# Performance work log

Measured on AMD Instinct MI355X. Metric: run time of the kernel, lower is better.

Reference implementation:

```python
import jax, jax.numpy as jnp
import numpy as np

N_NODES = 100000
N_EDGES = 3200000
D_IN = 256
D_OUT = 256


def setup_inputs() -> dict:
    key = jax.random.key(0)
    k1, k2, k3, k4, k5, k6 = jax.random.split(key, 6)
    x = jax.random.normal(k1, (N_NODES, D_IN), dtype=jnp.float32)
    edge_src = jax.random.randint(k2, (N_EDGES,), 0, N_NODES, dtype=jnp.int32)
    edge_dst = jax.random.randint(k3, (N_EDGES,), 0, N_NODES, dtype=jnp.int32)
    edge_weight = jax.random.uniform(k4, (N_EDGES,), dtype=jnp.float32)
    weight = jax.random.normal(k5, (D_IN, D_OUT), dtype=jnp.float32) * 0.02
    bias = jax.random.uniform(k6, (D_OUT,), dtype=jnp.float32)
    return {"x": x, "edge_src": edge_src, "edge_dst": edge_dst,
            "edge_weight": edge_weight, "weight": weight, "bias": bias}


def reference(x, edge_src, edge_dst, edge_weight, weight, bias):
    # support = X @ W  (dense GEMM)
    support = x @ weight  # [N, D_OUT]
    # output = A @ support, A given as COO edges (dst <- src with weight)
    msgs = support[edge_src] * edge_weight[:, None]  # [E, D_OUT]
    out = jax.ops.segment_sum(msgs, edge_dst, num_segments=N_NODES)  # [N, D_OUT]
    return out + bias
```

## Files before the change

### kernel.cpp

```cpp
#include <hip/hip_runtime.h>
#include <hip/hip_bf16.h>

#define N_NODES 100000
#define N_EDGES 3200000
#define DDIM    256
#define M_PAD   100096
#define NBKT    782
#define BCAP    4608
#define EPB_A   4096

typedef __attribute__((ext_vector_type(8))) short short8;
typedef __attribute__((ext_vector_type(4))) float f32x4;

typedef const __attribute__((address_space(1))) void gvoid_t;
typedef __attribute__((address_space(3))) void lvoid_t;

__device__ __forceinline__ void load_lds16(const void* g, void* l) {
  __builtin_amdgcn_global_load_lds((gvoid_t*)g, (lvoid_t*)l, 16, 0, 0);
}

__device__ __forceinline__ unsigned short f2bf(float f) {
  __hip_bfloat16 h = __float2bfloat16(f);
  return *(unsigned short*)&h;
}
__device__ __forceinline__ float bflo(unsigned u) { return __uint_as_float(u << 16); }
__device__ __forceinline__ float bfhi(unsigned u) { return __uint_as_float(u & 0xffff0000u); }

__global__ void conv_x_kernel(const float* __restrict__ x, unsigned short* __restrict__ xb) {
  size_t i = (size_t)blockIdx.x * blockDim.x + threadIdx.x;
  size_t idx = i * 4;
  if (idx >= (size_t)N_NODES * DDIM) return;
  float4 v = *(const float4*)(x + idx);
  ushort4 o;
  o.x = f2bf(v.x); o.y = f2bf(v.y); o.z = f2bf(v.z); o.w = f2bf(v.w);
  *(ushort4*)(xb + idx) = o;
}

__global__ void conv_w_kernel(const float* __restrict__ w, unsigned short* __restrict__ wt) {
  int t = blockIdx.x * blockDim.x + threadIdx.x;
  int n = t >> 8, k = t & 255;
  wt[t] = f2bf(w[k * 256 + n]);
}

__global__ __launch_bounds__(256) void gemm_kernel(const unsigned short* __restrict__ xb,
                                                   const unsigned short* __restrict__ wt,
                                                   unsigned short* __restrict__ sup) {
  __shared__ unsigned short As[128 * 32];
  __shared__ unsigned short Bs[128 * 32];
  const int tid  = threadIdx.x;
  const int w    = tid >> 6;
  const int lane = tid & 63;
  const int quad = lane >> 4;
  const int l15  = lane & 15;
  const int wr   = w >> 1, wc = w & 1;
  const int m0 = blockIdx.x * 128;
  const int n0 = blockIdx.y * 128;

  f32x4 acc[4][4] = {};

  const int srow   = lane >> 2;
  const int schunk = (lane & 3) * 8;

  for (int kt = 0; kt < 256; kt += 32) {
#pragma unroll
    for (int i = 0; i < 2; ++i) {
      int r = w * 32 + i * 16 + srow;
      load_lds16(xb + ((size_t)(m0 + r) * 256 + kt + schunk),
                 As + (w * 32 + i * 16) * 32);
      load_lds16(wt + ((size_t)(n0 + r) * 256 + kt + schunk),
                 Bs + (w * 32 + i * 16) * 32);
    }
    __syncthreads();

    short8 a[4], b[4];
#pragma unroll
    for (int mi = 0; mi < 4; ++mi)
      a[mi] = *(const short8*)(As + (wr * 64 + mi * 16 + l15) * 32 + quad * 8);
#pragma unroll
    for (int ni = 0; ni < 4; ++ni)
      b[ni] = *(const short8*)(Bs + (wc * 64 + ni * 16 + l15) * 32 + quad * 8);

#pragma unroll
    for (int mi = 0; mi < 4; ++mi)
#pragma unroll
      for (int ni = 0; ni < 4; ++ni)
        acc[mi][ni] = __builtin_amdgcn_mfma_f32_16x16x32_bf16(a[mi], b[ni], acc[mi][ni], 0, 0, 0);
    __syncthreads();
  }

#pragma unroll
  for (int mi = 0; mi < 4; ++mi) {
#pragma unroll
    for (int r = 0; r < 4; ++r) {
      size_t row = (size_t)(m0 + wr * 64 + mi * 16 + quad * 4 + r);
#pragma unroll
      for (int ni = 0; ni < 4; ++ni) {
        int col = n0 + wc * 64 + ni * 16 + l15;
        sup[row * 256 + col] = f2bf(acc[mi][ni][r]);
      }
    }
  }
}

__global__ __launch_bounds__(256) void binA_kernel(const int* __restrict__ src,
                                                   const int* __restrict__ dst,
                                                   const float* __restrict__ wgt,
                                                   int* __restrict__ gcur,
                                                   unsigned long long* __restrict__ region) {
  __shared__ unsigned long long staged[EPB_A];
  __shared__ unsigned short sbkt[EPB_A];
  __shared__ int lhist[NBKT];
  __shared__ int lstart[NBKT];
  __shared__ int lcur[NBKT];
  __shared__ int gb[NBKT];
  __shared__ int csum[256];

  const int t = threadIdx.x;
  const int e0 = blockIdx.x * EPB_A;
  const int ecnt = min(EPB_A, N_EDGES - e0);

  for (int i = t; i < NBKT; i += 256) lhist[i] = 0;
  __syncthreads();
  for (int k = t; k < ecnt; k += 256)
    atomicAdd(&lhist[dst[e0 + k] >> 7], 1);
  __syncthreads();

  int i0 = 4 * t;
  int a0 = (i0 + 0 < NBKT) ? lhist[i0 + 0] : 0;
  int a1 = (i0 + 1 < NBKT) ? lhist[i0 + 1] : 0;
  int a2 = (i0 + 2 < NBKT) ? lhist[i0 + 2] : 0;
  int a3 = (i0 + 3 < NBKT) ? lhist[i0 + 3] : 0;
  int s = a0 + a1 + a2 + a3;
  csum[t] = s;
  __syncthreads();
  for (int off = 1; off < 256; off <<= 1) {
    int v = (t >= off) ? csum[t - off] : 0;
    __syncthreads();
    csum[t] += v;
    __syncthreads();
  }
  int base = csum[t] - s;
  if (i0 + 0 < NBKT) lstart[i0 + 0] = base; base += a0;
  if (i0 + 1 < NBKT) lstart[i0 + 1] = base; base += a1;
  if (i0 + 2 < NBKT) lstart[i0 + 2] = base; base += a2;
  if (i0 + 3 < NBKT) lstart[i0 + 3] = base;
  __syncthreads();

  for (int i = t; i < NBKT; i += 256) {
    int c = lhist[i];
    int off = c ? atomicAdd(&gcur[i], c) : 0;
    gb[i] = i * BCAP + off;
    lcur[i] = lstart[i];
  }
  __syncthreads();

  for (int k = t; k < ecnt; k += 256) {
    int d  = dst[e0 + k];
    int sr = src[e0 + k];
    float w = wgt[e0 + k];
    int b = d >> 7;
    int p = atomicAdd(&lcur[b], 1);
    staged[p] = ((unsigned long long)__float_as_uint(w) << 32) |
                ((unsigned)(d & 127) << 17) | (unsigned)sr;
    sbkt[p] = (unsigned short)b;
  }
  __syncthreads();

  for (int j = t; j < ecnt; j += 256) {
    int b = sbkt[j];
    int addr = gb[b] + (j - lstart[b]);
    if (addr < (b + 1) * BCAP) region[addr] = staged[j];
  }
}

__global__ __launch_bounds__(256) void csrB_kernel(unsigned long long* __restrict__ region,
                                                   const int* __restrict__ gcur,
                                                   int2* __restrict__ rowse) {
  __shared__ unsigned long long lcsr[BCAP];
  __shared__ int lhist[128], loff[128], lcur[128];
  const int t = threadIdx.x;
  const int b = blockIdx.x;
  const int cnt = min(gcur[b], BCAP);
  const int base = b * BCAP;

  if (t < 128) lhist[t] = 0;
  __syncthreads();
  for (int j = t; j < cnt; j += 256) {
    unsigned lo = (unsigned)(region[base + j] & 0xffffffffu);
    atomicAdd(&lhist[(lo >> 17) & 127], 1);
  }
  __syncthreads();
  if (t < 128) loff[t] = lhist[t];
  __syncthreads();
  for (int off = 1; off < 128; off <<= 1) {
    int v = (t >= off && t < 128) ? loff[t - off] : 0;
    __syncthreads();
    if (t < 128) loff[t] += v;
    __syncthreads();
  }
  if (t < 128) { loff[t] -= lhist[t]; lcur[t] = loff[t]; }
  __syncthreads();
  for (int j = t; j < cnt; j += 256) {
    unsigned long long e = region[base + j];
    int dl = (int)((e >> 17) & 127);
    int p = atomicAdd(&lcur[dl], 1);
    lcsr[p] = e;
  }
  __syncthreads();
  for (int j = t; j < cnt; j += 256) region[base + j] = lcsr[j];
  if (t < 128) {
    int gd = b * 128 + t;
    if (gd < N_NODES) rowse[gd] = make_int2(base + loff[t], base + lcur[t]);
  }
}

__global__ __launch_bounds__(64) void gather_kernel(const unsigned long long* __restrict__ packed,
                                                    const int2* __restrict__ rowse,
                                                    const unsigned short* __restrict__ sup,
                                                    const float* __restrict__ bias,
                                                    float* __restrict__ out) {
  int n = blockIdx.x;
  int l = threadIdx.x;
  int c0 = l * 4;
  int2 se = rowse[n];
  int start = se.x, end = se.y;
  float4 bv = *(const float4*)(bias + c0);
  float a0 = bv.x, a1 = bv.y, a2 = bv.z, a3 = bv.w;

  int i = start;
  for (; i + 2 <= end; i += 2) {
    unsigned long long m0 = packed[i];
    unsigned long long m1 = packed[i + 1];
    int   s0 = (int)(m0 & 0x1ffffu);
    float w0 = __uint_as_float((unsigned)(m0 >> 32));
    int   s1 = (int)(m1 & 0x1ffffu);
    float w1 = __uint_as_float((unsigned)(m1 >> 32));
    uint2 p0 = *(const uint2*)(sup + (size_t)s0 * 256 + c0);
    uint2 p1 = *(const uint2*)(sup + (size_t)s1 * 256 + c0);
    a0 = fmaf(w0, bflo(p0.x), a0);
    a1 = fmaf(w0, bfhi(p0.x), a1);
    a2 = fmaf(w0, bflo(p0.y), a2);
    a3 = fmaf(w0, bfhi(p0.y), a3);
    a0 = fmaf(w1, bflo(p1.x), a0);
    a1 = fmaf(w1, bfhi(p1.x), a1);
    a2 = fmaf(w1, bflo(p1.y), a2);
    a3 = fmaf(w1, bfhi(p1.y), a3);
  }
  if (i < end) {
    unsigned long long m0 = packed[i];
    int   s0 = (int)(m0 & 0x1ffffu);
    float w0 = __uint_as_float((unsigned)(m0 >> 32));
    uint2 p0 = *(const uint2*)(sup + (size_t)s0 * 256 + c0);
    a0 = fmaf(w0, bflo(p0.x), a0);
    a1 = fmaf(w0, bfhi(p0.x), a1);
    a2 = fmaf(w0, bflo(p0.y), a2);
    a3 = fmaf(w0, bfhi(p0.y), a3);
  }
  *(float4*)(out + (size_t)n * 256 + c0) = make_float4(a0, a1, a2, a3);
}

extern "C" void kernel_launch(void* const* d_in, const int* in_sizes, int n_in,
                              void* d_out, int out_size, void* d_ws, size_t ws_size,
                              hipStream_t stream) {
  const float* x        = (const float*)d_in[0];
  const int*   edge_src = (const int*)d_in[1];
  const int*   edge_dst = (const int*)d_in[2];
  const float* edge_w   = (const float*)d_in[3];
  const float* weight   = (const float*)d_in[4];
  const float* bias     = (const float*)d_in[5];
  float* out = (float*)d_out;

  char* ws = (char*)d_ws;
  size_t off = 0;
  auto alloc = [&](size_t bytes) -> void* {
    void* p = ws + off;
    off = (off + bytes + 255) & ~(size_t)255;
    return p;
  };

  unsigned short* xb  = (unsigned short*)alloc((size_t)M_PAD * 256 * 2);
  unsigned short* wt  = (unsigned short*)alloc(256 * 256 * 2);
  unsigned short* sup = (unsigned short*)alloc((size_t)M_PAD * 256 * 2);

  char* xbb = (char*)xb;
  unsigned long long* region = (unsigned long long*)xbb;
  int*  gcur  = (int*)(xbb + (29u << 20));
  int2* rowse = (int2*)(xbb + (30u << 20));

  conv_x_kernel<<<25000, 256, 0, stream>>>(x, xb);
  conv_w_kernel<<<256, 256, 0, stream>>>(weight, wt);
  gemm_kernel<<<dim3(782, 2), 256, 0, stream>>>(xb, wt, sup);
  hipMemsetAsync(gcur, 0, NBKT * 4, stream);
  binA_kernel<<<(N_EDGES + EPB_A - 1) / EPB_A, 256, 0, stream>>>(edge_src, edge_dst, edge_w,
                                                                 gcur, region);
  csrB_kernel<<<NBKT, 256, 0, stream>>>(region, gcur, rowse);
  gather_kernel<<<N_NODES, 64, 0, stream>>>(region, rowse, sup, bias, out);
}
```

Baseline: 532.8 us.

## Fuse per-bucket CSR sort with the neighbor gather using the LDS-resident edge list

Merges the CSR bucket sort and the gather into one kernel with 512-thread blocks. Each block sorts its bucket's edges in LDS, then its 8 waves each aggregate 16 destination nodes straight from the LDS-sorted list. This drops the sorted-edge write-back, the row start/end array, one kernel launch and the global re-read of edges. The cost is a much smaller grid (782 blocks instead of 100k single-wave blocks), which may lower latency hiding for the random support reads and add load imbalance across waves.

Result: no change. 531.1 us (-0.3%).

```diff
diff --git a/kernel.cpp b/kernel.cpp
--- a/kernel.cpp
+++ b/kernel.cpp
@@ -8,6 +8,7 @@
 #define NBKT    782
 #define BCAP    4608
 #define EPB_A   4096
+#define GT      512
 
 typedef __attribute__((ext_vector_type(8))) short short8;
 typedef __attribute__((ext_vector_type(4))) float f32x4;
@@ -173,9 +174,12 @@
   }
 }
 
-__global__ __launch_bounds__(256) void csrB_kernel(unsigned long long* __restrict__ region,
-                                                   const int* __restrict__ gcur,
-                                                   int2* __restrict__ rowse) {
+__global__ __launch_bounds__(GT) void csr_gather_kernel(
+    const unsigned long long* __restrict__ region,
+    const int* __restrict__ gcur,
+    const unsigned short* __restrict__ sup,
+    const float* __restrict__ bias,
+    float* __restrict__ out) {
   __shared__ unsigned long long lcsr[BCAP];
   __shared__ int lhist[128], loff[128], lcur[128];
   const int t = threadIdx.x;
@@ -185,7 +189,7 @@
 
   if (t < 128) lhist[t] = 0;
   __syncthreads();
-  for (int j = t; j < cnt; j += 256) {
+  for (int j = t; j < cnt; j += GT) {
     unsigned lo = (unsigned)(region[base + j] & 0xffffffffu);
     atomicAdd(&lhist[(lo >> 17) & 127], 1);
   }
@@ -200,63 +204,56 @@
   }
   if (t < 128) { loff[t] -= lhist[t]; lcur[t] = loff[t]; }
   __syncthreads();
-  for (int j = t; j < cnt; j += 256) {
+  for (int j = t; j < cnt; j += GT) {
     unsigned long long e = region[base + j];
     int dl = (int)((e >> 17) & 127);
     int p = atomicAdd(&lcur[dl], 1);
     lcsr[p] = e;
   }
   __syncthreads();
-  for (int j = t; j < cnt; j += 256) region[base + j] = lcsr[j];
-  if (t < 128) {
-    int gd = b * 128 + t;
-    if (gd < N_NODES) rowse[gd] = make_int2(base + loff[t], base + lcur[t]);
-  }
-}
-
-__global__ __launch_bounds__(64) void gather_kernel(const unsigned long long* __restrict__ packed,
-                                                    const int2* __restrict__ rowse,
-                                                    const unsigned short* __restrict__ sup,
-                                                    const float* __restrict__ bias,
-                                                    float* __restrict__ out) {
-  int n = blockIdx.x;
-  int l = threadIdx.x;
-  int c0 = l * 4;
-  int2 se = rowse[n];
-  int start = se.x, end = se.y;
+
+  const int wv = t >> 6;
+  const int c0 = (t & 63) * 4;
   float4 bv = *(const float4*)(bias + c0);
-  float a0 = bv.x, a1 = bv.y, a2 = bv.z, a3 = bv.w;
-
-  int i = start;
-  for (; i + 2 <= end; i += 2) {
-    unsigned long long m0 = packed[i];
-    unsigned long long m1 = packed[i + 1];
-    int   s0 = (int)(m0 & 0x1ffffu);
-    float w0 = __uint_as_float((unsigned)(m0 >> 32));
-    int   s1 = (int)(m1 & 0x1ffffu);
-    float w1 = __uint_as_float((unsigned)(m1 >> 32));
-    uint2 p0 = *(const uint2*)(sup + (size_t)s0 * 256 + c0);
-    uint2 p1 = *(const uint2*)(sup + (size_t)s1 * 256 + c0);
-    a0 = fmaf(w0, bflo(p0.x), a0);
-    a1 = fmaf(w0, bfhi(p0.x), a1);
-    a2 = fmaf(w0, bflo(p0.y), a2);
-    a3 = fmaf(w0, bfhi(p0.y), a3);
-    a0 = fmaf(w1, bflo(p1.x), a0);
-    a1 = fmaf(w1, bfhi(p1.x), a1);
-    a2 = fmaf(w1, bflo(p1.y), a2);
-    a3 = fmaf(w1, bfhi(p1.y), a3);
-  }
-  if (i < end) {
-    unsigned long long m0 = packed[i];
-    int   s0 = (int)(m0 & 0x1ffffu);
-    float w0 = __uint_as_float((unsigned)(m0 >> 32));
-    uint2 p0 = *(const uint2*)(sup + (size_t)s0 * 256 + c0);
-    a0 = fmaf(w0, bflo(p0.x), a0);
-    a1 = fmaf(w0, bfhi(p0.x), a1);
-    a2 = fmaf(w0, bflo(p0.y), a2);
-    a3 = fmaf(w0, bfhi(p0.y), a3);
-  }
-  *(float4*)(out + (size_t)n * 256 + c0) = make_float4(a0, a1, a2, a3);
+
+  for (int dl = wv; dl < 128; dl += 8) {
+    int node = b * 128 + dl;
+    if (node >= N_NODES) continue;
+    int start = loff[dl];
+    int end   = lcur[dl];
+    float a0 = bv.x, a1 = bv.y, a2 = bv.z, a3 = bv.w;
+
+    int i = start;
+    for (; i + 2 <= end; i += 2) {
+      unsigned long long m0 = lcsr[i];
+      unsigned long long m1 = lcsr[i + 1];
+      int   s0 = (int)(m0 & 0x1ffffu);
+      float w0 = __uint_as_float((unsigned)(m0 >> 32));
+      int   s1 = (int)(m1 & 0x1ffffu);
+      float w1 = __uint_as_float((unsigned)(m1 >> 32));
+      uint2 p0 = *(const uint2*)(sup + (size_t)s0 * 256 + c0);
+      uint2 p1 = *(const uint2*)(sup + (size_t)s1 * 256 + c0);
+      a0 = fmaf(w0, bflo(p0.x), a0);
+      a1 = fmaf(w0, bfhi(p0.x), a1);
+      a2 = fmaf(w0, bflo(p0.y), a2);
+      a3 = fmaf(w0, bfhi(p0.y), a3);
+      a0 = fmaf(w1, bflo(p1.x), a0);
+      a1 = fmaf(w1, bfhi(p1.x), a1);
+      a2 = fmaf(w1, bflo(p1.y), a2);
+      a3 = fmaf(w1, bfhi(p1.y), a3);
+    }
+    if (i < end) {
+      unsigned long long m0 = lcsr[i];
+      int   s0 = (int)(m0 & 0x1ffffu);
+      float w0 = __uint_as_float((unsigned)(m0 >> 32));
+      uint2 p0 = *(const uint2*)(sup + (size_t)s0 * 256 + c0);
+      a0 = fmaf(w0, bflo(p0.x), a0);
+      a1 = fmaf(w0, bfhi(p0.x), a1);
+      a2 = fmaf(w0, bflo(p0.y), a2);
+      a3 = fmaf(w0, bfhi(p0.y), a3);
+    }
+    *(float4*)(out + (size_t)node * 256 + c0) = make_float4(a0, a1, a2, a3);
+  }
 }
 
 extern "C" void kernel_launch(void* const* d_in, const int* in_sizes, int n_in,
@@ -285,7 +282,6 @@
   char* xbb = (char*)xb;
   unsigned long long* region = (unsigned long long*)xbb;
   int*  gcur  = (int*)(xbb + (29u << 20));
-  int2* rowse = (int2*)(xbb + (30u << 20));
 
   conv_x_kernel<<<25000, 256, 0, stream>>>(x, xb);
   conv_w_kernel<<<256, 256, 0, stream>>>(weight, wt);
@@ -293,6 +289,5 @@
   hipMemsetAsync(gcur, 0, NBKT * 4, stream);
   binA_kernel<<<(N_EDGES + EPB_A - 1) / EPB_A, 256, 0, stream>>>(edge_src, edge_dst, edge_w,
                                                                  gcur, region);
-  csrB_kernel<<<NBKT, 256, 0, stream>>>(region, gcur, rowse);
-  gather_kernel<<<N_NODES, 64, 0, stream>>>(region, rowse, sup, bias, out);
-}
+  csr_gather_kernel<<<NBKT, GT, 0, stream>>>(region, gcur, sup, bias, out);
+}
```
